# Kernel optimization log

Hardware: AMD Instinct MI355X
Metric: run time of the kernel (lower is better)

Reference implementation:

```python
import jax, jax.numpy as jnp
import numpy as np

L, T, H, F = 16, 2048, 2048, 512  # layers, tokens (B*S=16*128), hidden, features


def setup_inputs() -> dict:
    key = jax.random.key(0)
    k1, k2, k3 = jax.random.split(key, 3)
    x = jax.random.normal(k1, (L, T, H), dtype=jnp.float32)          # stacked residual activations
    W_enc = jax.random.normal(k2, (L, F, H), dtype=jnp.float32) * 0.02  # per-layer encoder (out,in)
    # Dense pack of decoders: W_dec[s, t] is the (source s -> target t) decoder weight (H, F).
    # Only entries with s <= t exist in the original ModuleDict; others are masked to zero in reference().
    W_dec = jax.random.normal(k3, (L, L, H, F), dtype=jnp.float32) * 0.02
    return {"x": x, "W_enc": W_enc, "W_dec": W_dec}


def reference(x, W_enc, W_dec):
    n_layers = x.shape[0]
    # encode: feature_activations[l] = JumpReLU(x[l] @ W_enc[l].T), threshold=0 -> relu
    feats = jax.nn.relu(jnp.einsum('sth,sfh->stf', x, W_enc))  # [L, T, F]
    # causal mask over (source s, target l): decoder exists iff s <= l
    tri = jnp.tril(jnp.ones((n_layers, n_layers), x.dtype))     # tri[l, s] = 1 if s <= l
    Wd = W_dec * tri.T[:, :, None, None]                        # zero out s > l entries
    # reconstruction[l] = sum_{s<=l} feats[s] @ W_dec[s,l].T  (single blocked contraction)
    recon = jnp.einsum('stf,slhf->lth', feats, Wd)              # [L, T, H]
    return feats, recon
```

## Files before the change

kernel.cpp:

```cpp
#include <hip/hip_runtime.h>

#define NL 16
#define NT 2048
#define NH 2048
#define NF 512
#define NPAIR 136

typedef short bf16x8 __attribute__((ext_vector_type(8)));
typedef float f32x16 __attribute__((ext_vector_type(16)));
typedef short s16x4 __attribute__((ext_vector_type(4)));

__device__ __forceinline__ short f2bf(float f) {
  union { float f; unsigned u; } x; x.f = f;
  unsigned r = (x.u + 0x7fffu + ((x.u >> 16) & 1u)) >> 16;
  return (short)r;
}

__device__ __forceinline__ int imin(int a, int b) { return a < b ? a : b; }


__global__ void k_cvt_f32_bf16(const float* __restrict__ src, short* __restrict__ dst, int n4) {
  int i = blockIdx.x * blockDim.x + threadIdx.x;
  const int stride = gridDim.x * blockDim.x;
  for (; i < n4; i += stride) {
    const float4 v = reinterpret_cast<const float4*>(src)[i];
    s16x4 o;
    o[0] = f2bf(v.x); o[1] = f2bf(v.y); o[2] = f2bf(v.z); o[3] = f2bf(v.w);
    reinterpret_cast<s16x4*>(dst)[i] = o;
  }
}

__global__ void k_cvt_wdec(const float* __restrict__ wdec, short* __restrict__ dst) {
  const int p = blockIdx.y;
  int l = 0;
  while ((l + 1) * (l + 2) / 2 <= p) ++l;
  const int s = p - l * (l + 1) / 2;
  const float* src = wdec + (size_t)(s * NL + l) * (NH * NF);
  short* d = dst + (size_t)p * (NH * NF);
  const int n4 = NH * NF / 4;
  for (int i = blockIdx.x * blockDim.x + threadIdx.x; i < n4; i += gridDim.x * blockDim.x) {
    const float4 v = reinterpret_cast<const float4*>(src)[i];
    s16x4 o;
    o[0] = f2bf(v.x); o[1] = f2bf(v.y); o[2] = f2bf(v.z); o[3] = f2bf(v.w);
    reinterpret_cast<s16x4*>(d)[i] = o;
  }
}


__device__ __forceinline__ bf16x8 lds_frag(const short* slot, int r, int cbyte) {
  int byte = (r << 7) + cbyte;
  byte ^= (r & 7) << 4;
  return *reinterpret_cast<const bf16x8*>(reinterpret_cast<const char*>(slot) + byte);
}

__device__ __forceinline__ void stage_half(short* slot, const short* gbase, int ld,
                                           int isA, int h, int tid, int wave) {
#pragma unroll
  for (int j = 0; j < 2; ++j) {
    const int o = j * 8192 + tid * 16;
    const int r = o >> 7;
    const int cb = (o ^ ((r & 7) << 4)) & 127;
    const int g = isA ? (((r >> 6) << 7) + h * 64 + (r & 63))
                      : (((r >> 5) << 6) + h * 32 + (r & 31));
    __builtin_amdgcn_global_load_lds(
        (const __attribute__((address_space(1))) void*)(gbase + (size_t)g * ld + (cb >> 1)),
        (__attribute__((address_space(3))) void*)((char*)slot + j * 8192 + wave * 1024),
        16, 0, 0);
  }
}

__device__ __forceinline__ void phase_end() {
  asm volatile("s_waitcnt vmcnt(8)" ::: "memory");
  __builtin_amdgcn_s_barrier();
}

template <typename S0, typename S1, typename S2, typename S3>
__device__ __forceinline__ void ktile(short (*bufc)[8192], f32x16 (&acc)[4][2],
                                      int wr, int wc, int lane,
                                      S0 s0, S1 s1, S2 s2, S3 s3) {
  const int rl = lane & 31;
  const int khi = (lane >> 5) * 16;
  bf16x8 aA[4][2], aB[4][2], b0[4], b1[4];
  s0();
#pragma unroll
  for (int ks = 0; ks < 4; ++ks) {
    aA[ks][0] = lds_frag(bufc[0], wr * 64 + rl, ks * 32 + khi);
    aA[ks][1] = lds_frag(bufc[0], wr * 64 + 32 + rl, ks * 32 + khi);
    b0[ks] = lds_frag(bufc[2], wc * 32 + rl, ks * 32 + khi);
  }
  __builtin_amdgcn_s_setprio(1);
#pragma unroll
  for (int ks = 0; ks < 4; ++ks) {
    acc[0][0] = __builtin_amdgcn_mfma_f32_32x32x16_bf16(aA[ks][0], b0[ks], acc[0][0], 0, 0, 0);
    acc[1][0] = __builtin_amdgcn_mfma_f32_32x32x16_bf16(aA[ks][1], b0[ks], acc[1][0], 0, 0, 0);
  }
  __builtin_amdgcn_s_setprio(0);
  phase_end();
  s1();
#pragma unroll
  for (int ks = 0; ks < 4; ++ks)
    b1[ks] = lds_frag(bufc[3], wc * 32 + rl, ks * 32 + khi);
  __builtin_amdgcn_s_setprio(1);
#pragma unroll
  for (int ks = 0; ks < 4; ++ks) {
    acc[0][1] = __builtin_amdgcn_mfma_f32_32x32x16_bf16(aA[ks][0], b1[ks], acc[0][1], 0, 0, 0);
    acc[1][1] = __builtin_amdgcn_mfma_f32_32x32x16_bf16(aA[ks][1], b1[ks], acc[1][1], 0, 0, 0);
  }
  __builtin_amdgcn_s_setprio(0);
  phase_end();
  s2();
#pragma unroll
  for (int ks = 0; ks < 4; ++ks) {
    aB[ks][0] = lds_frag(bufc[1], wr * 64 + rl, ks * 32 + khi);
    aB[ks][1] = lds_frag(bufc[1], wr * 64 + 32 + rl, ks * 32 + khi);
  }
  __builtin_amdgcn_s_setprio(1);
#pragma unroll
  for (int ks = 0; ks < 4; ++ks) {
    acc[2][0] = __builtin_amdgcn_mfma_f32_32x32x16_bf16(aB[ks][0], b0[ks], acc[2][0], 0, 0, 0);
    acc[3][0] = __builtin_amdgcn_mfma_f32_32x32x16_bf16(aB[ks][1], b0[ks], acc[3][0], 0, 0, 0);
  }
  __builtin_amdgcn_s_setprio(0);
  phase_end();
  s3();
  __builtin_amdgcn_s_setprio(1);
#pragma unroll
  for (int ks = 0; ks < 4; ++ks) {
    acc[2][1] = __builtin_amdgcn_mfma_f32_32x32x16_bf16(aB[ks][0], b1[ks], acc[2][1], 0, 0, 0);
    acc[3][1] = __builtin_amdgcn_mfma_f32_32x32x16_bf16(aB[ks][1], b1[ks], acc[3][1], 0, 0, 0);
  }
  __builtin_amdgcn_s_setprio(0);
  phase_end();
}


__global__ __launch_bounds__(512, 2) void k_encode256(const short* __restrict__ xbf,
                                                      const short* __restrict__ webf,
                                                      float* __restrict__ feats_f32,
                                                      short* __restrict__ feats_bf) {
  __shared__ short lds[2][4][8192];
  const int l = blockIdx.z;
  const int row0 = blockIdx.y * 256;
  const int col0 = blockIdx.x * 256;
  const int tid = threadIdx.x;
  const int wave = tid >> 6, lane = tid & 63;
  const int wr = wave >> 2, wc = wave & 3;

  const short* A = xbf + (size_t)l * NT * NH + (size_t)row0 * NH;
  const short* B = webf + (size_t)l * NF * NH + (size_t)col0 * NH;

  f32x16 acc[4][2];
#pragma unroll
  for (int tm = 0; tm < 4; ++tm)
#pragma unroll
    for (int tn = 0; tn < 2; ++tn)
#pragma unroll
      for (int q = 0; q < 16; ++q) acc[tm][tn][q] = 0.f;

  const int KT = NH / 64;
  stage_half(lds[0][0], A, NH, 1, 0, tid, wave);
  stage_half(lds[0][2], B, NH, 0, 0, tid, wave);
  stage_half(lds[0][1], A, NH, 1, 1, tid, wave);
  stage_half(lds[0][3], B, NH, 0, 1, tid, wave);
  stage_half(lds[1][0], A + 64, NH, 1, 0, tid, wave);
  stage_half(lds[1][2], B + 64, NH, 0, 0, tid, wave);
  asm volatile("s_waitcnt vmcnt(4)" ::: "memory");
  __builtin_amdgcn_s_barrier();

  for (int u = 0; u < KT; ++u) {
    short(*bufc)[8192] = lds[u & 1];
    short(*bufn)[8192] = lds[(u + 1) & 1];
    ktile(bufc, acc, wr, wc, lane,
          [&] { stage_half(bufn[3], B + imin(u + 1, KT - 1) * 64, NH, 0, 1, tid, wave); },
          [&] { stage_half(bufn[1], A + imin(u + 1, KT - 1) * 64, NH, 1, 1, tid, wave); },
          [&] { stage_half(bufc[0], A + imin(u + 2, KT - 1) * 64, NH, 1, 0, tid, wave); },
          [&] { stage_half(bufc[2], B + imin(u + 2, KT - 1) * 64, NH, 0, 0, tid, wave); });
  }

  const int rl = lane & 31, lhi = (lane >> 5) * 4;
  float* outF = feats_f32 + (size_t)l * NT * NF;
  short* outB = feats_bf + (size_t)l * NT * NF;
#pragma unroll
  for (int tm = 0; tm < 4; ++tm)
#pragma unroll
    for (int tn = 0; tn < 2; ++tn)
#pragma unroll
      for (int q = 0; q < 16; ++q) {
        const int rr = row0 + wr * 128 + tm * 32 + (q & 3) + 8 * (q >> 2) + lhi;
        const int cc = col0 + wc * 64 + tn * 32 + rl;
        float v = acc[tm][tn][q];
        v = v > 0.f ? v : 0.f;
        outF[(size_t)rr * NF + cc] = v;
        outB[(size_t)rr * NF + cc] = f2bf(v);
      }
}


__global__ __launch_bounds__(512, 2) void k_decode256(const short* __restrict__ featsbf,
                                                      const short* __restrict__ wdbf,
                                                      float* __restrict__ recon) {
  __shared__ short lds[2][4][8192];
  const int l = (NL - 1) - blockIdx.z;
  const int row0 = blockIdx.y * 256;
  const int col0 = blockIdx.x * 256;
  const int tid = threadIdx.x;
  const int wave = tid >> 6, lane = tid & 63;
  const int wr = wave >> 2, wc = wave & 3;
  const int pbase = l * (l + 1) / 2;

  const short* Af = featsbf + (size_t)row0 * NF;
  const short* Bw = wdbf + (size_t)col0 * NF;

  f32x16 acc[4][2];
#pragma unroll
  for (int tm = 0; tm < 4; ++tm)
#pragma unroll
    for (int tn = 0; tn < 2; ++tn)
#pragma unroll
      for (int q = 0; q < 16; ++q) acc[tm][tn][q] = 0.f;

  const int KT = 8 * (l + 1);
#define ABASE(kt) (Af + (size_t)((kt) >> 3) * (NT * NF) + ((kt)&7) * 64)
#define BBASE(kt) (Bw + (size_t)(pbase + ((kt) >> 3)) * (NH * NF) + ((kt)&7) * 64)

  stage_half(lds[0][0], ABASE(0), NF, 1, 0, tid, wave);
  stage_half(lds[0][2], BBASE(0), NF, 0, 0, tid, wave);
  stage_half(lds[0][1], ABASE(0), NF, 1, 1, tid, wave);
  stage_half(lds[0][3], BBASE(0), NF, 0, 1, tid, wave);
  stage_half(lds[1][0], ABASE(1), NF, 1, 0, tid, wave);
  stage_half(lds[1][2], BBASE(1), NF, 0, 0, tid, wave);
  asm volatile("s_waitcnt vmcnt(4)" ::: "memory");
  __builtin_amdgcn_s_barrier();

  for (int u = 0; u < KT; ++u) {
    short(*bufc)[8192] = lds[u & 1];
    short(*bufn)[8192] = lds[(u + 1) & 1];
    ktile(bufc, acc, wr, wc, lane,
          [&] { stage_half(bufn[3], BBASE(imin(u + 1, KT - 1)), NF, 0, 1, tid, wave); },
          [&] { stage_half(bufn[1], ABASE(imin(u + 1, KT - 1)), NF, 1, 1, tid, wave); },
          [&] { stage_half(bufc[0], ABASE(imin(u + 2, KT - 1)), NF, 1, 0, tid, wave); },
          [&] { stage_half(bufc[2], BBASE(imin(u + 2, KT - 1)), NF, 0, 0, tid, wave); });
  }
#undef ABASE
#undef BBASE

  const int rl = lane & 31, lhi = (lane >> 5) * 4;
  float* out = recon + (size_t)l * NT * NH;
#pragma unroll
  for (int tm = 0; tm < 4; ++tm)
#pragma unroll
    for (int tn = 0; tn < 2; ++tn)
#pragma unroll
      for (int q = 0; q < 16; ++q) {
        const int rr = row0 + wr * 128 + tm * 32 + (q & 3) + 8 * (q >> 2) + lhi;
        const int cc = col0 + wc * 64 + tn * 32 + rl;
        out[(size_t)rr * NH + cc] = acc[tm][tn][q];
      }
}


extern "C" void kernel_launch(void* const* d_in, const int* in_sizes, int n_in,
                              void* d_out, int out_size, void* d_ws, size_t ws_size,
                              hipStream_t stream) {
  const float* x = (const float*)d_in[0];
  const float* wenc = (const float*)d_in[1];
  const float* wdec = (const float*)d_in[2];

  float* feats_f32 = (float*)d_out;
  float* recon = feats_f32 + (size_t)NL * NT * NF;

  short* x_bf = (short*)d_ws;
  short* we_bf = x_bf + (size_t)NL * NT * NH;
  short* wd_bf = we_bf + (size_t)NL * NF * NH;
  short* ft_bf = wd_bf + (size_t)NPAIR * NH * NF;

  k_cvt_f32_bf16<<<2048, 256, 0, stream>>>(x, x_bf, NL * NT * NH / 4);
  k_cvt_f32_bf16<<<2048, 256, 0, stream>>>(wenc, we_bf, NL * NF * NH / 4);
  k_cvt_wdec<<<dim3(512, NPAIR), 256, 0, stream>>>(wdec, wd_bf);

  k_encode256<<<dim3(2, 8, 16), 512, 0, stream>>>(x_bf, we_bf, feats_f32, ft_bf);
  k_decode256<<<dim3(8, 8, 16), 512, 0, stream>>>(ft_bf, wd_bf, recon);
}
```

Before: 926.7 us.

## Use 16x16x32 MFMA in encoder and remap grids to 1D swizzled block order

The encoder's K-tile loop now uses 16x16x32 bf16 MFMA instructions with 4-wide accumulators instead of 32x32x16, with a matching epilogue index mapping. Both encoder and decoder launches become 1D grids whose block index is decoded into (layer, row, col) in a swizzled order, aiming for better L2 reuse of shared tiles across neighbouring blocks. The 16x16 MFMA variant may offer different throughput or LDS fragment patterns, but it issues more instructions per tile and changes register pressure.

```diff
diff --git a/kernel.cpp b/kernel.cpp
--- a/kernel.cpp
+++ b/kernel.cpp
@@ -7,6 +7,7 @@
 #define NPAIR 136
 
 typedef short bf16x8 __attribute__((ext_vector_type(8)));
+typedef float f32x4 __attribute__((ext_vector_type(4)));
 typedef float f32x16 __attribute__((ext_vector_type(16)));
 typedef short s16x4 __attribute__((ext_vector_type(4)));
 
@@ -75,9 +76,85 @@
 }
 
 template <typename S0, typename S1, typename S2, typename S3>
-__device__ __forceinline__ void ktile(short (*bufc)[8192], f32x16 (&acc)[4][2],
-                                      int wr, int wc, int lane,
-                                      S0 s0, S1 s1, S2 s2, S3 s3) {
+__device__ __forceinline__ void ktile16(short (*bufc)[8192], f32x4 (&acc)[2][2][4][2],
+                                        int wr, int wc, int lane,
+                                        S0 s0, S1 s1, S2 s2, S3 s3) {
+  const int lr = lane & 15;
+  const int ko = (lane >> 4) * 16;
+  bf16x8 a0[2][4], a1[2][4], b0[2][2], b1[2][2];
+  s0();
+#pragma unroll
+  for (int kk = 0; kk < 2; ++kk) {
+#pragma unroll
+    for (int m = 0; m < 4; ++m)
+      a0[kk][m] = lds_frag(bufc[0], wr * 64 + m * 16 + lr, kk * 64 + ko);
+#pragma unroll
+    for (int n = 0; n < 2; ++n)
+      b0[kk][n] = lds_frag(bufc[2], wc * 32 + n * 16 + lr, kk * 64 + ko);
+  }
+  __builtin_amdgcn_s_setprio(1);
+#pragma unroll
+  for (int kk = 0; kk < 2; ++kk)
+#pragma unroll
+    for (int m = 0; m < 4; ++m)
+#pragma unroll
+      for (int n = 0; n < 2; ++n)
+        acc[0][0][m][n] = __builtin_amdgcn_mfma_f32_16x16x32_bf16(a0[kk][m], b0[kk][n],
+                                                                  acc[0][0][m][n], 0, 0, 0);
+  __builtin_amdgcn_s_setprio(0);
+  phase_end();
+  s1();
+#pragma unroll
+  for (int kk = 0; kk < 2; ++kk)
+#pragma unroll
+    for (int n = 0; n < 2; ++n)
+      b1[kk][n] = lds_frag(bufc[3], wc * 32 + n * 16 + lr, kk * 64 + ko);
+  __builtin_amdgcn_s_setprio(1);
+#pragma unroll
+  for (int kk = 0; kk < 2; ++kk)
+#pragma unroll
+    for (int m = 0; m < 4; ++m)
+#pragma unroll
+      for (int n = 0; n < 2; ++n)
+        acc[0][1][m][n] = __builtin_amdgcn_mfma_f32_16x16x32_bf16(a0[kk][m], b1[kk][n],
+                                                                  acc[0][1][m][n], 0, 0, 0);
+  __builtin_amdgcn_s_setprio(0);
+  phase_end();
+  s2();
+#pragma unroll
+  for (int kk = 0; kk < 2; ++kk)
+#pragma unroll
+    for (int m = 0; m < 4; ++m)
+      a1[kk][m] = lds_frag(bufc[1], wr * 64 + m * 16 + lr, kk * 64 + ko);
+  __builtin_amdgcn_s_setprio(1);
+#pragma unroll
+  for (int kk = 0; kk < 2; ++kk)
+#pragma unroll
+    for (int m = 0; m < 4; ++m)
+#pragma unroll
+      for (int n = 0; n < 2; ++n)
+        acc[1][0][m][n] = __builtin_amdgcn_mfma_f32_16x16x32_bf16(a1[kk][m], b0[kk][n],
+                                                                  acc[1][0][m][n], 0, 0, 0);
+  __builtin_amdgcn_s_setprio(0);
+  phase_end();
+  s3();
+  __builtin_amdgcn_s_setprio(1);
+#pragma unroll
+  for (int kk = 0; kk < 2; ++kk)
+#pragma unroll
+    for (int m = 0; m < 4; ++m)
+#pragma unroll
+      for (int n = 0; n < 2; ++n)
+        acc[1][1][m][n] = __builtin_amdgcn_mfma_f32_16x16x32_bf16(a1[kk][m], b1[kk][n],
+                                                                  acc[1][1][m][n], 0, 0, 0);
+  __builtin_amdgcn_s_setprio(0);
+  phase_end();
+}
+
+template <typename S0, typename S1, typename S2, typename S3>
+__device__ __forceinline__ void ktile32(short (*bufc)[8192], f32x16 (&acc)[4][2],
+                                        int wr, int wc, int lane,
+                                        S0 s0, S1 s1, S2 s2, S3 s3) {
   const int rl = lane & 31;
   const int khi = (lane >> 5) * 16;
   bf16x8 aA[4][2], aB[4][2], b0[4], b1[4];
@@ -139,9 +216,11 @@
                                                       float* __restrict__ feats_f32,
                                                       short* __restrict__ feats_bf) {
   __shared__ short lds[2][4][8192];
-  const int l = blockIdx.z;
-  const int row0 = blockIdx.y * 256;
-  const int col0 = blockIdx.x * 256;
+  const int d = blockIdx.x;
+  const int p = ((d >> 6) << 3) | (d & 7);
+  const int l = p >> 1;
+  const int row0 = ((d >> 3) & 7) * 256;
+  const int col0 = (p & 1) * 256;
   const int tid = threadIdx.x;
   const int wave = tid >> 6, lane = tid & 63;
   const int wr = wave >> 2, wc = wave & 3;
@@ -149,13 +228,18 @@
   const short* A = xbf + (size_t)l * NT * NH + (size_t)row0 * NH;
   const short* B = webf + (size_t)l * NF * NH + (size_t)col0 * NH;
 
-  f32x16 acc[4][2];
-#pragma unroll
-  for (int tm = 0; tm < 4; ++tm)
-#pragma unroll
-    for (int tn = 0; tn < 2; ++tn)
-#pragma unroll
-      for (int q = 0; q < 16; ++q) acc[tm][tn][q] = 0.f;
+  f32x4 acc[2][2][4][2];
+#pragma unroll
+  for (int qa = 0; qa < 2; ++qa)
+#pragma unroll
+    for (int qb = 0; qb < 2; ++qb)
+#pragma unroll
+      for (int m = 0; m < 4; ++m)
+#pragma unroll
+        for (int n = 0; n < 2; ++n) {
+          f32x4 z = {0.f, 0.f, 0.f, 0.f};
+          acc[qa][qb][m][n] = z;
+        }
 
   const int KT = NH / 64;
   stage_half(lds[0][0], A, NH, 1, 0, tid, wave);
@@ -170,29 +254,33 @@
   for (int u = 0; u < KT; ++u) {
     short(*bufc)[8192] = lds[u & 1];
     short(*bufn)[8192] = lds[(u + 1) & 1];
-    ktile(bufc, acc, wr, wc, lane,
-          [&] { stage_half(bufn[3], B + imin(u + 1, KT - 1) * 64, NH, 0, 1, tid, wave); },
-          [&] { stage_half(bufn[1], A + imin(u + 1, KT - 1) * 64, NH, 1, 1, tid, wave); },
-          [&] { stage_half(bufc[0], A + imin(u + 2, KT - 1) * 64, NH, 1, 0, tid, wave); },
-          [&] { stage_half(bufc[2], B + imin(u + 2, KT - 1) * 64, NH, 0, 0, tid, wave); });
-  }
-
-  const int rl = lane & 31, lhi = (lane >> 5) * 4;
+    ktile16(bufc, acc, wr, wc, lane,
+            [&] { stage_half(bufn[3], B + imin(u + 1, KT - 1) * 64, NH, 0, 1, tid, wave); },
+            [&] { stage_half(bufn[1], A + imin(u + 1, KT - 1) * 64, NH, 1, 1, tid, wave); },
+            [&] { stage_half(bufc[0], A + imin(u + 2, KT - 1) * 64, NH, 1, 0, tid, wave); },
+            [&] { stage_half(bufc[2], B + imin(u + 2, KT - 1) * 64, NH, 0, 0, tid, wave); });
+  }
+
+  const int lr4 = (lane >> 4) * 4, lc = lane & 15;
   float* outF = feats_f32 + (size_t)l * NT * NF;
   short* outB = feats_bf + (size_t)l * NT * NF;
 #pragma unroll
-  for (int tm = 0; tm < 4; ++tm)
-#pragma unroll
-    for (int tn = 0; tn < 2; ++tn)
-#pragma unroll
-      for (int q = 0; q < 16; ++q) {
-        const int rr = row0 + wr * 128 + tm * 32 + (q & 3) + 8 * (q >> 2) + lhi;
-        const int cc = col0 + wc * 64 + tn * 32 + rl;
-        float v = acc[tm][tn][q];
-        v = v > 0.f ? v : 0.f;
-        outF[(size_t)rr * NF + cc] = v;
-        outB[(size_t)rr * NF + cc] = f2bf(v);
-      }
+  for (int qa = 0; qa < 2; ++qa)
+#pragma unroll
+    for (int qb = 0; qb < 2; ++qb)
+#pragma unroll
+      for (int m = 0; m < 4; ++m)
+#pragma unroll
+        for (int n = 0; n < 2; ++n)
+#pragma unroll
+          for (int rg = 0; rg < 4; ++rg) {
+            const int rr = row0 + wr * 128 + qa * 64 + m * 16 + lr4 + rg;
+            const int cc = col0 + wc * 64 + qb * 32 + n * 16 + lc;
+            float v = acc[qa][qb][m][n][rg];
+            v = v > 0.f ? v : 0.f;
+            outF[(size_t)rr * NF + cc] = v;
+            outB[(size_t)rr * NF + cc] = f2bf(v);
+          }
 }
 
 
@@ -200,9 +288,10 @@
                                                       const short* __restrict__ wdbf,
                                                       float* __restrict__ recon) {
   __shared__ short lds[2][4][8192];
-  const int l = (NL - 1) - blockIdx.z;
-  const int row0 = blockIdx.y * 256;
-  const int col0 = blockIdx.x * 256;
+  const int d = blockIdx.x;
+  const int l = 15 - (d >> 6);
+  const int row0 = ((d >> 3) & 7) * 256;
+  const int col0 = (d & 7) * 256;
   const int tid = threadIdx.x;
   const int wave = tid >> 6, lane = tid & 63;
   const int wr = wave >> 2, wc = wave & 3;
@@ -235,11 +324,11 @@
   for (int u = 0; u < KT; ++u) {
     short(*bufc)[8192] = lds[u & 1];
     short(*bufn)[8192] = lds[(u + 1) & 1];
-    ktile(bufc, acc, wr, wc, lane,
-          [&] { stage_half(bufn[3], BBASE(imin(u + 1, KT - 1)), NF, 0, 1, tid, wave); },
-          [&] { stage_half(bufn[1], ABASE(imin(u + 1, KT - 1)), NF, 1, 1, tid, wave); },
-          [&] { stage_half(bufc[0], ABASE(imin(u + 2, KT - 1)), NF, 1, 0, tid, wave); },
-          [&] { stage_half(bufc[2], BBASE(imin(u + 2, KT - 1)), NF, 0, 0, tid, wave); });
+    ktile32(bufc, acc, wr, wc, lane,
+            [&] { stage_half(bufn[3], BBASE(imin(u + 1, KT - 1)), NF, 0, 1, tid, wave); },
+            [&] { stage_half(bufn[1], ABASE(imin(u + 1, KT - 1)), NF, 1, 1, tid, wave); },
+            [&] { stage_half(bufc[0], ABASE(imin(u + 2, KT - 1)), NF, 1, 0, tid, wave); },
+            [&] { stage_half(bufc[2], BBASE(imin(u + 2, KT - 1)), NF, 0, 0, tid, wave); });
   }
 #undef ABASE
 #undef BBASE
@@ -278,6 +367,6 @@
   k_cvt_f32_bf16<<<2048, 256, 0, stream>>>(wenc, we_bf, NL * NF * NH / 4);
   k_cvt_wdec<<<dim3(512, NPAIR), 256, 0, stream>>>(wdec, wd_bf);
 
-  k_encode256<<<dim3(2, 8, 16), 512, 0, stream>>>(x_bf, we_bf, feats_f32, ft_bf);
-  k_decode256<<<dim3(8, 8, 16), 512, 0, stream>>>(ft_bf, wd_bf, recon);
-}
+  k_encode256<<<256, 512, 0, stream>>>(x_bf, we_bf, feats_f32, ft_bf);
+  k_decode256<<<1024, 512, 0, stream>>>(ft_bf, wd_bf, recon);
+}
```

After: 902.5 us. -2.6%, faster.
